# Optimization experiments

Measured on AMD Instinct MI355X. Metric: run time of the kernel, lower is better.

## Reference

```python
import jax, jax.numpy as jnp
import numpy as np

N, E, H = 50000, 800000, 128
NUM_NC = 40
NUM_LAYERS = 3


def setup_inputs() -> dict:
    key = jax.random.key(0)
    ks = jax.random.split(key, 16)
    s = 1.0 / np.sqrt(H)
    inp = {
        "x": jax.random.normal(ks[0], (N, H), jnp.float32),
        "edge_index": jax.random.randint(ks[1], (2, E), 0, N, jnp.int64),
        "na_alphas": 0.001 * jax.random.normal(ks[2], (3, 4), jnp.float32),
        "sc_alphas": 0.001 * jax.random.normal(ks[3], (2, 2), jnp.float32),
        "la_alphas": 0.001 * jax.random.normal(ks[4], (1, 3), jnp.float32),
        "lin1_W": s * jax.random.normal(ks[5], (H, H), jnp.float32),
        "lin1_b": jnp.zeros((H,), jnp.float32),
        "gcn_W": s * jax.random.normal(ks[6], (3, H, H), jnp.float32),
        "gcn_b": jnp.zeros((3, H), jnp.float32),
        "sage_Ws": s * jax.random.normal(ks[7], (3, H, H), jnp.float32),
        "sage_Wn": s * jax.random.normal(ks[8], (3, H, H), jnp.float32),
        "gin_W": s * jax.random.normal(ks[9], (3, H, H), jnp.float32),
        "gin_b": jnp.zeros((3, H), jnp.float32),
        "gin_eps": jnp.zeros((3,), jnp.float32),
        "gat_W": s * jax.random.normal(ks[10], (3, H, H), jnp.float32),
        "gat_as": s * jax.random.normal(ks[11], (3, H), jnp.float32),
        "gat_ad": s * jax.random.normal(ks[12], (3, H), jnp.float32),
        "nc_W": s * jax.random.normal(ks[13], (NUM_NC, H), jnp.float32),
        "nc_b": jnp.zeros((NUM_NC,), jnp.float32),
    }
    return inp


def _gcn(x, src, dst, deg_inv_sqrt, W, b):
    h = x @ W.T + b                           # [N, H]
    norm = deg_inv_sqrt[src] * deg_inv_sqrt[dst]
    msg = h[src] * norm[:, None]              # [E, H] gather
    return jax.ops.segment_sum(msg, dst, num_segments=N)


def _sage(x, src, dst, deg, Ws, Wn):
    agg = jax.ops.segment_sum(x[src], dst, num_segments=N) / jnp.maximum(deg, 1.0)[:, None]
    return x @ Ws.T + agg @ Wn.T


def _gin(x, src, dst, W, b, eps):
    agg = jax.ops.segment_sum(x[src], dst, num_segments=N)
    return ((1.0 + eps) * x + agg) @ W.T + b


def _gat(x, src, dst, W, a_s, a_d):
    h = x @ W.T                               # [N, H]
    logits = jax.nn.leaky_relu((h @ a_s)[src] + (h @ a_d)[dst], 0.2)  # [E]
    m = jax.ops.segment_max(logits, dst, num_segments=N)
    e = jnp.exp(logits - m[dst])
    z = jax.ops.segment_sum(e, dst, num_segments=N)
    alpha = e / (z[dst] + 1e-16)
    return jax.ops.segment_sum(alpha[:, None] * h[src], dst, num_segments=N)


def _na_mixed(x, w, src, dst, deg, dis, l, gcn_W, gcn_b, sage_Ws, sage_Wn,
              gin_W, gin_b, gin_eps, gat_W, gat_as, gat_ad):
    # sum_i w_i * elu(op_i(x, edge_index))
    o0 = _gcn(x, src, dst, dis, gcn_W[l], gcn_b[l])
    o1 = _sage(x, src, dst, deg, sage_Ws[l], sage_Wn[l])
    o2 = _gin(x, src, dst, gin_W[l], gin_b[l], gin_eps[l])
    o3 = _gat(x, src, dst, gat_W[l], gat_as[l], gat_ad[l])
    return (w[0] * jax.nn.elu(o0) + w[1] * jax.nn.elu(o1)
            + w[2] * jax.nn.elu(o2) + w[3] * jax.nn.elu(o3))


def reference(x, edge_index, na_alphas, sc_alphas, la_alphas, lin1_W, lin1_b,
              gcn_W, gcn_b, sage_Ws, sage_Wn, gin_W, gin_b, gin_eps,
              gat_W, gat_as, gat_ad, nc_W, nc_b):
    src, dst = edge_index[0], edge_index[1]
    deg = jax.ops.segment_sum(jnp.ones((E,), x.dtype), dst, num_segments=N)
    dis = jnp.where(deg > 0, 1.0 / jnp.sqrt(jnp.maximum(deg, 1.0)), 0.0)

    na_w = jax.nn.softmax(na_alphas, axis=-1)   # [3, 4]
    sc_w = jax.nn.softmax(sc_alphas, axis=-1)   # [2, 2] (none, skip)
    la_w = jax.nn.softmax(la_alphas, axis=-1)   # [1, 3]

    h = x @ lin1_W.T + lin1_b                   # dropout: eval mode -> identity
    xs = []
    cur = h
    for l in range(NUM_LAYERS):
        cur = _na_mixed(cur, na_w[l], src, dst, deg, dis, l, gcn_W, gcn_b,
                        sage_Ws, sage_Wn, gin_W, gin_b, gin_eps,
                        gat_W, gat_as, gat_ad)
        xs.append(cur)
    x1, x2, x3 = xs

    # fix_last=True: x4 = (x3, sc0(x1), sc1(x2)); SC ops = {none->0, skip->id}
    t = jnp.stack([x3, sc_w[0, 1] * x1, sc_w[1, 1] * x2], axis=0)  # [3, N, H]

    # layer aggregator: sum_i w_i * relu(op_i(tuple)); ops = {max, mean, sum}
    x5 = (la_w[0, 0] * jax.nn.relu(jnp.max(t, axis=0))
          + la_w[0, 1] * jax.nn.relu(jnp.mean(t, axis=0))
          + la_w[0, 2] * jax.nn.relu(jnp.sum(t, axis=0)))

    return x5 @ nc_W.T + nc_b                   # [N, NUM_NC]
```

## Files before the change

kernel.cpp:

```cpp
#include <hip/hip_runtime.h>
#include <hip/hip_bf16.h>

typedef unsigned short u16;
typedef unsigned int u32;
typedef __attribute__((ext_vector_type(8))) short short8;
typedef __attribute__((ext_vector_type(4))) float f32x4;
typedef __attribute__((ext_vector_type(2))) float f32x2;

#define HD 128
#define ETILE 8192

__device__ inline float b2f(u16 u){ u32 v = ((u32)u) << 16; return __uint_as_float(v); }
__device__ inline u16 f2b(float f){
  u32 u = __float_as_uint(f);
  u32 r = (u + 0x7fffu + ((u >> 16) & 1u)) >> 16;
  return (u16)r;
}
__device__ inline u32 pack2(float a, float b){
  __hip_bfloat162 h = __float22bfloat162_rn(make_float2(a, b));
  union { __hip_bfloat162 h; u32 u; } c; c.h = h; return c.u;
}
__device__ inline float lo2f(u32 w){ return b2f((u16)(w & 0xffff)); }
__device__ inline float hi2f(u32 w){ return b2f((u16)(w >> 16)); }
__device__ inline float eluf(float x){ return x > 0.f ? x : __expf(x) - 1.f; }
__device__ inline float reluf(float x){ return x > 0.f ? x : 0.f; }
__device__ inline float sane(float x){
  if (!(x == x)) return 0.f;
  return fminf(fmaxf(x, -1e30f), 1e30f);
}
__device__ inline u32 fenc(float f){ u32 u = __float_as_uint(f); return (u & 0x80000000u) ? ~u : (u | 0x80000000u); }
__device__ inline float fdec(u32 u){ return __uint_as_float((u & 0x80000000u) ? (u & 0x7fffffffu) : ~u); }
__device__ __forceinline__ void async16(const u16* g, u16* l){
  __builtin_amdgcn_global_load_lds((const __attribute__((address_space(1))) void*)g,
                                   (__attribute__((address_space(3))) void*)l, 16, 0, 0);
}

__global__ void k_small(const float* __restrict__ na_a, const float* __restrict__ sc_a,
                        const float* __restrict__ la_a, const float* __restrict__ gatW,
                        const float* __restrict__ gat_as, const float* __restrict__ gat_ad,
                        const float* __restrict__ gin_eps, float* __restrict__ sm,
                        u32* __restrict__ maxs)
{
  int t = threadIdx.x;
  if (t < 3) maxs[t] = 0u;
  if (t == 0){
    for (int l = 0; l < 3; l++){
      float a[4]; float mx = -1e30f;
      for (int i = 0; i < 4; i++){ a[i] = na_a[l*4+i]; mx = fmaxf(mx, a[i]); }
      float ssum = 0.f;
      for (int i = 0; i < 4; i++){ a[i] = __expf(a[i]-mx); ssum += a[i]; }
      for (int i = 0; i < 4; i++) sm[l*4+i] = a[i]/ssum;
    }
    for (int r = 0; r < 2; r++){
      float a0 = sc_a[r*2], a1 = sc_a[r*2+1];
      float mx = fmaxf(a0,a1);
      float e0 = __expf(a0-mx), e1 = __expf(a1-mx);
      sm[12+r] = e1/(e0+e1);
    }
    {
      float a0=la_a[0], a1=la_a[1], a2=la_a[2];
      float mx = fmaxf(fmaxf(a0,a1),a2);
      float e0=__expf(a0-mx), e1=__expf(a1-mx), e2=__expf(a2-mx);
      float ssum = e0+e1+e2;
      sm[14]=e0/ssum; sm[15]=e1/ssum; sm[16]=e2/ssum;
    }
    for (int l=0;l<3;l++) sm[17+l] = 1.f + gin_eps[l];
  }
  if (t < 128){
    for (int l=0;l<3;l++){
      float a1=0.f, a2=0.f;
      for (int k=0;k<128;k++){
        float wv = gatW[l*16384 + k*128 + t];
        a1 = fmaf(wv, gat_as[l*128+k], a1);
        a2 = fmaf(wv, gat_ad[l*128+k], a2);
      }
      sm[32  + l*128 + t] = a1;
      sm[416 + l*128 + t] = a2;
    }
  }
}

__device__ __forceinline__ uint4 cvt8(const float* __restrict__ p){
  float4 v0 = *(const float4*)p;
  float4 v1 = *(const float4*)(p + 4);
  uint4 o;
  o.x = pack2(v0.x, v0.y);
  o.y = pack2(v0.z, v0.w);
  o.z = pack2(v1.x, v1.y);
  o.w = pack2(v1.z, v1.w);
  return o;
}
__global__ void k_wcvt(const float* __restrict__ lin1W, const float* __restrict__ gcnW,
                       const float* __restrict__ Ws, const float* __restrict__ Wn,
                       const float* __restrict__ ginW, const float* __restrict__ gatW,
                       u16* __restrict__ wsb)
{
  int i = blockIdx.x*256 + threadIdx.x;
  if (i >= 32768) return;
  int m = i >> 11;
  int j = i & 2047;
  int r = j >> 4, c = j & 15;
  const float* src;
  if (m == 0)       src = lin1W;
  else if (m < 4)   src = gcnW + (m-1)*16384;
  else if (m < 7)   src = Ws   + (m-4)*16384;
  else if (m < 10)  src = Wn   + (m-7)*16384;
  else if (m < 13)  src = ginW + (m-10)*16384;
  else              src = gatW + (m-13)*16384;
  int dj = r*16 + (c ^ (r & 15));
  *(uint4*)(wsb + ((size_t)m*2048 + dj)*8) = cvt8(src + r*HD + c*8);
}


__global__ void k_ehist(const int* __restrict__ ei, int E, int* __restrict__ eh){
  __shared__ int h[256];
  int t = threadIdx.x, b = blockIdx.x;
  h[t] = 0; __syncthreads();
  int base = b*ETILE;
  #pragma unroll
  for (int r = 0; r < ETILE/256; r++){
    int e = base + r*256 + t;
    if (e < E) atomicAdd(&h[ei[E + e] >> 8], 1);
  }
  __syncthreads();
  eh[b*256 + t] = h[t];
}
__global__ void k_escan(int* __restrict__ eh, int nblk, int* __restrict__ btot){
  __shared__ int s[256];
  int b = blockIdx.x, t = threadIdx.x;
  int carry = 0;
  int rounds = (nblk + 255)/256;
  for (int r = 0; r < rounds; r++){
    int i = r*256 + t;
    int v = (i < nblk) ? eh[i*256 + b] : 0;
    s[t] = v; __syncthreads();
    for (int off = 1; off < 256; off <<= 1){
      int a = (t >= off) ? s[t - off] : 0;
      __syncthreads();
      s[t] += a;
      __syncthreads();
    }
    if (i < nblk) eh[i*256 + b] = s[t] - v + carry;
    carry += s[255];
    __syncthreads();
  }
  if (t == 0) btot[b] = carry;
}
__global__ void k_bscan(const int* __restrict__ btot, int B, int E, int* __restrict__ bbase){
  __shared__ int s[256];
  int t = threadIdx.x;
  int v = (t < B) ? btot[t] : 0;
  s[t] = v; __syncthreads();
  for (int off = 1; off < 256; off <<= 1){
    int a = (t >= off) ? s[t - off] : 0;
    __syncthreads();
    s[t] += a;
    __syncthreads();
  }
  if (t < B) bbase[t] = s[t] - v;
  if (t == 0) bbase[B] = E;
}
__global__ void k_escat(const int* __restrict__ ei, int E, int B,
                        const int* __restrict__ eh, const int* __restrict__ bbase,
                        int2* __restrict__ ebuf){
  __shared__ int cur[256];
  int t = threadIdx.x, b = blockIdx.x;
  cur[t] = (t < B) ? bbase[t] + eh[b*256 + t] : 0;
  __syncthreads();
  int base = b*ETILE;
  #pragma unroll
  for (int r = 0; r < ETILE/256; r++){
    int e = base + r*256 + t;
    if (e < E){
      int sv = ei[e], dv = ei[E + e];
      int p = atomicAdd(&cur[dv >> 8], 1);
      ebuf[p] = make_int2(sv, dv);
    }
  }
}
__global__ void k_bcount(const int2* __restrict__ ebuf, const int* __restrict__ bbase,
                         int Nn, int* __restrict__ cnt){
  __shared__ int c[256];
  int t = threadIdx.x, b = blockIdx.x;
  c[t] = 0; __syncthreads();
  int beg = bbase[b], end2 = bbase[b+1];
  for (int i = beg + t; i < end2; i += 256)
    atomicAdd(&c[ebuf[i].y & 255], 1);
  __syncthreads();
  int node = b*256 + t;
  if (node < Nn) cnt[node] = c[t];
}
__global__ void k_bfill(const int2* __restrict__ ebuf, const int* __restrict__ bbase,
                        const int* __restrict__ rowptr, int Nn, int* __restrict__ csr){
  __shared__ int cu[256];
  int t = threadIdx.x, b = blockIdx.x;
  int node = b*256 + t;
  cu[t] = (node < Nn) ? rowptr[node] : 0;
  __syncthreads();
  int beg = bbase[b], end2 = bbase[b+1];
  for (int i = beg + t; i < end2; i += 256){
    int2 ed = ebuf[i];
    int p = atomicAdd(&cu[ed.y & 255], 1);
    csr[p] = ed.x;
  }
}

__global__ void k_scan1(const int* __restrict__ cnt, int Nn, int* __restrict__ bsum){
  __shared__ int red[256];
  int b = blockIdx.x, t = threadIdx.x;
  int base = b*1024 + t*4;
  int s = 0;
  #pragma unroll
  for (int k = 0; k < 4; k++){ int i = base + k; if (i < Nn) s += cnt[i]; }
  red[t] = s; __syncthreads();
  for (int off = 128; off; off >>= 1){
    if (t < off) red[t] += red[t + off];
    __syncthreads();
  }
  if (t == 0) bsum[b] = red[0];
}

__global__ void k_scan2(const int* __restrict__ bsum, int nb,
                        int* __restrict__ boffs, int* __restrict__ rowptr, int Nn){
  __shared__ int sc[1024];
  int t = threadIdx.x;
  int own = (t < nb) ? bsum[t] : 0;
  sc[t] = own;
  __syncthreads();
  for (int off = 1; off < 1024; off <<= 1){
    int add = (t >= off) ? sc[t - off] : 0;
    __syncthreads();
    sc[t] += add;
    __syncthreads();
  }
  if (t < nb) boffs[t] = sc[t] - own;
  if (t == 1023) rowptr[Nn] = sc[1023];
}

__global__ void k_scan3(const int* __restrict__ cnt, const int* __restrict__ boffs, int Nn,
                        int* __restrict__ rowptr, float4* __restrict__ nd){
  __shared__ int red[256];
  int b = blockIdx.x, t = threadIdx.x;
  int base = b*1024 + t*4;
  int c[4]; int s = 0;
  #pragma unroll
  for (int k = 0; k < 4; k++){ int i = base + k; c[k] = (i < Nn) ? cnt[i] : 0; s += c[k]; }
  red[t] = s; __syncthreads();
  for (int off = 1; off < 256; off <<= 1){
    int add = (t >= off) ? red[t - off] : 0;
    __syncthreads();
    red[t] += add;
    __syncthreads();
  }
  int run = red[t] - s + boffs[b];
  #pragma unroll
  for (int k = 0; k < 4; k++){
    int i = base + k;
    if (i < Nn){
      rowptr[i] = run;
      float f = (float)c[k];
      nd[i].z = c[k] > 0 ? 1.f/sqrtf(f) : 0.f;
      nd[i].w = 1.f/fmaxf(f, 1.f);
      run += c[k];
    }
  }
}

__global__ void k_histblk(const int* __restrict__ cnt, int Nn, int* __restrict__ bh){
  __shared__ int h[256];
  int t = threadIdx.x, b = blockIdx.x;
  h[t] = 0; __syncthreads();
  int base = b*1024;
  #pragma unroll
  for (int k = 0; k < 4; k++){
    int i = base + t + k*256;
    if (i < Nn){ int d = cnt[i]; if (d > 255) d = 255; atomicAdd(&h[d], 1); }
  }
  __syncthreads();
  bh[b*256 + t] = h[t];
}
__global__ void k_hsscan(int* __restrict__ bh, int nb){
  __shared__ int tot[256];
  __shared__ int sc[256];
  int t = threadIdx.x;
  int s = 0;
  for (int b = 0; b < nb; b++){
    int v = bh[b*256 + t];
    bh[b*256 + t] = s;
    s += v;
  }
  tot[t] = s;
  int rt = 255 - t;
  __syncthreads();
  sc[rt] = tot[t];
  __syncthreads();
  for (int off = 1; off < 256; off <<= 1){
    int a = (rt >= off) ? sc[rt - off] : 0;
    __syncthreads();
    sc[rt] += a;
    __syncthreads();
  }
  int binbase = sc[rt] - tot[t];
  for (int b = 0; b < nb; b++) bh[b*256 + t] += binbase;
}
__global__ void k_permscat(const int* __restrict__ cnt, int Nn,
                           const int* __restrict__ bh, int* __restrict__ perm){
  __shared__ int cur[256];
  int t = threadIdx.x, b = blockIdx.x;
  cur[t] = bh[b*256 + t];
  __syncthreads();
  int base = b*1024;
  #pragma unroll
  for (int k = 0; k < 4; k++){
    int i = base + t + k*256;
    if (i < Nn){
      int d = cnt[i]; if (d > 255) d = 255;
      int p = atomicAdd(&cur[d], 1);
      perm[p] = i;
    }
  }
}

__global__ __launch_bounds__(256)
void k_agg(const u16* __restrict__ X, const int* __restrict__ rowptr, const int* __restrict__ csr,
           const int* __restrict__ perm,
           const float4* __restrict__ nd, const float* __restrict__ sm,
           const u32* __restrict__ maxs, int layer, int Nn,
           u16* __restrict__ Qb, u16* __restrict__ Pm, u16* __restrict__ Gb, u16* __restrict__ Rb,
           float* __restrict__ b0)
{
  int tid = threadIdx.x;
  int lane = tid & 63;
  int g = lane >> 4, t = lane & 15;
  int idx = blockIdx.x*16 + (tid >> 6)*4 + g;
  if (idx >= Nn) return;
  int wv = perm[idx];
  int beg = rowptr[wv], end = rowptr[wv+1];
  float4 ndw = nd[wv];
  float dval = ndw.y;
  float bnd = fdec(maxs[layer]) + dval;
  float mloc = fmaxf(bnd, 0.2f*bnd);
  f32x2 p2[4], q2[4], r2[4];
  #pragma unroll
  for (int k = 0; k < 4; k++){ p2[k] = (f32x2){0.f,0.f}; q2[k] = (f32x2){0.f,0.f}; r2[k] = (f32x2){0.f,0.f}; }
  float z = 0.f, qd = 0.f;
  int e = beg;
  int nsv0=0, nsv1=0, nsv2=0, nsv3=0;
  if (e + 3 < end){ nsv0 = csr[e]; nsv1 = csr[e+1]; nsv2 = csr[e+2]; nsv3 = csr[e+3]; }
  while (e + 3 < end){
    int sv0 = nsv0, sv1 = nsv1, sv2 = nsv2, sv3 = nsv3;
    int en = e + 4;
    if (en + 3 < end){ nsv0 = csr[en]; nsv1 = csr[en+1]; nsv2 = csr[en+2]; nsv3 = csr[en+3]; }
    float4 n0 = nd[sv0], n1 = nd[sv1], n2 = nd[sv2], n3 = nd[sv3];
    uint4 xv0 = *(const uint4*)(X + (size_t)sv0*HD + (t ^ (sv0 & 15))*8);
    uint4 xv1 = *(const uint4*)(X + (size_t)sv1*HD + (t ^ (sv1 & 15))*8);
    uint4 xv2 = *(const uint4*)(X + (size_t)sv2*HD + (t ^ (sv2 & 15))*8);
    uint4 xv3 = *(const uint4*)(X + (size_t)sv3*HD + (t ^ (sv3 & 15))*8);
    float s0 = n0.x + dval, s1 = n1.x + dval, s2 = n2.x + dval, s3 = n3.x + dval;
    float lg0 = fmaxf(s0, 0.2f*s0), lg1 = fmaxf(s1, 0.2f*s1);
    float lg2 = fmaxf(s2, 0.2f*s2), lg3 = fmaxf(s3, 0.2f*s3);
    float ew0 = __expf(lg0 - mloc), ew1 = __expf(lg1 - mloc);
    float ew2 = __expf(lg2 - mloc), ew3 = __expf(lg3 - mloc);
    u32 a0[4] = {xv0.x, xv0.y, xv0.z, xv0.w};
    u32 a1[4] = {xv1.x, xv1.y, xv1.z, xv1.w};
    u32 a2[4] = {xv2.x, xv2.y, xv2.z, xv2.w};
    u32 a3[4] = {xv3.x, xv3.y, xv3.z, xv3.w};
    f32x2 d0 = {n0.z, n0.z}, d1 = {n1.z, n1.z}, d2 = {n2.z, n2.z}, d3 = {n3.z, n3.z};
    f32x2 e0 = {ew0, ew0}, e1v = {ew1, ew1}, e2v = {ew2, ew2}, e3v = {ew3, ew3};
    #pragma unroll
    for (int k = 0; k < 4; k++){
      f32x2 xf0 = {lo2f(a0[k]), hi2f(a0[k])};
      f32x2 xf1 = {lo2f(a1[k]), hi2f(a1[k])};
      f32x2 xf2 = {lo2f(a2[k]), hi2f(a2[k])};
      f32x2 xf3 = {lo2f(a3[k]), hi2f(a3[k])};
      p2[k] += (xf0 + xf1) + (xf2 + xf3);
      q2[k] = __builtin_elementwise_fma(xf0, d0, q2[k]);
      q2[k] = __builtin_elementwise_fma(xf1, d1, q2[k]);
      q2[k] = __builtin_elementwise_fma(xf2, d2, q2[k]);
      q2[k] = __builtin_elementwise_fma(xf3, d3, q2[k]);
      r2[k] = __builtin_elementwise_fma(xf0, e0, r2[k]);
      r2[k] = __builtin_elementwise_fma(xf1, e1v, r2[k]);
      r2[k] = __builtin_elementwise_fma(xf2, e2v, r2[k]);
      r2[k] = __builtin_elementwise_fma(xf3, e3v, r2[k]);
    }
    z += (ew0 + ew1) + (ew2 + ew3);
    qd += (n0.z + n1.z) + (n2.z + n3.z);
    e = en;
  }
  if (e + 1 < end){
    int sv0 = csr[e], sv1 = csr[e+1];
    float4 n0 = nd[sv0], n1 = nd[sv1];
    uint4 xv0 = *(const uint4*)(X + (size_t)sv0*HD + (t ^ (sv0 & 15))*8);
    uint4 xv1 = *(const uint4*)(X + (size_t)sv1*HD + (t ^ (sv1 & 15))*8);
    float s0 = n0.x + dval, s1 = n1.x + dval;
    float lg0 = fmaxf(s0, 0.2f*s0);
    float lg1 = fmaxf(s1, 0.2f*s1);
    float ew0 = __expf(lg0 - mloc), ew1 = __expf(lg1 - mloc);
    u32 a0[4] = {xv0.x, xv0.y, xv0.z, xv0.w};
    u32 a1[4] = {xv1.x, xv1.y, xv1.z, xv1.w};
    f32x2 d0 = {n0.z, n0.z}, d1 = {n1.z, n1.z};
    f32x2 e0 = {ew0, ew0},   e1v = {ew1, ew1};
    #pragma unroll
    for (int k = 0; k < 4; k++){
      f32x2 xf0 = {lo2f(a0[k]), hi2f(a0[k])};
      f32x2 xf1 = {lo2f(a1[k]), hi2f(a1[k])};
      p2[k] += xf0 + xf1;
      q2[k] = __builtin_elementwise_fma(xf0, d0, q2[k]);
      q2[k] = __builtin_elementwise_fma(xf1, d1, q2[k]);
      r2[k] = __builtin_elementwise_fma(xf0, e0, r2[k]);
      r2[k] = __builtin_elementwise_fma(xf1, e1v, r2[k]);
    }
    z += ew0 + ew1; qd += n0.z + n1.z;
    e += 2;
  }
  if (e < end){
    int sv = csr[e];
    float4 n0 = nd[sv];
    uint4 xv = *(const uint4*)(X + (size_t)sv*HD + (t ^ (sv & 15))*8);
    float s = n0.x + dval;
    float lg = fmaxf(s, 0.2f*s);
    float ew = __expf(lg - mloc);
    u32 a0[4] = {xv.x, xv.y, xv.z, xv.w};
    f32x2 d0 = {n0.z, n0.z}, e0 = {ew, ew};
    #pragma unroll
    for (int k = 0; k < 4; k++){
      f32x2 xf = {lo2f(a0[k]), hi2f(a0[k])};
      p2[k] += xf;
      q2[k] = __builtin_elementwise_fma(xf, d0, q2[k]);
      r2[k] = __builtin_elementwise_fma(xf, e0, r2[k]);
    }
    z += ew; qd += n0.z;
  }
  {
    float disv = ndw.z, dinvv = ndw.w;
    float zinv = 1.f/(z + 1e-16f);
    float e1 = sm[17 + layer];
    int tch = t ^ (wv & 15);
    size_t o = (size_t)wv*HD + tch*8;
    uint4 xo = *(const uint4*)(X + o);
    u32 ax[4] = {xo.x, xo.y, xo.z, xo.w};
    uint4 qo, po, go, ro;
    u32* qp = (u32*)&qo; u32* pp = (u32*)&po; u32* gp = (u32*)&go; u32* rp = (u32*)&ro;
    #pragma unroll
    for (int k = 0; k < 4; k++){
      float x0 = lo2f(ax[k]), x1 = hi2f(ax[k]);
      qp[k] = pack2(disv*q2[k].x, disv*q2[k].y);
      pp[k] = pack2(dinvv*p2[k].x, dinvv*p2[k].y);
      gp[k] = pack2(fmaf(e1, x0, p2[k].x), fmaf(e1, x1, p2[k].y));
      rp[k] = pack2(zinv*r2[k].x, zinv*r2[k].y);
    }
    *(uint4*)(Qb + o) = qo;
    *(uint4*)(Pm + o) = po;
    *(uint4*)(Gb + o) = go;
    *(uint4*)(Rb + o) = ro;
    if (t == 0) b0[wv] = disv*qd;
  }
}

__device__ __forceinline__ void stageB_async(u16* lds, const u16* __restrict__ w, int tid){
  int lane = tid & 63, wave = tid >> 6;
  #pragma unroll
  for (int i = 0; i < 8; i++){
    int cb = wave*64 + 256*i;
    async16(w + (size_t)(cb + lane)*8, lds + (size_t)cb*8);
  }
}
__device__ __forceinline__ void stageA64_async(u16* lds, const u16* __restrict__ src,
                                               int mbase, int Nn, int tid){
  int lane = tid & 63, wave = tid >> 6;
  #pragma unroll
  for (int i = 0; i < 4; i++){
    int cb = wave*64 + 256*i;
    int gr = mbase + ((cb + lane) >> 4);
    if (gr < Nn)
      async16(src + ((size_t)mbase*16 + cb + lane)*8, lds + (size_t)cb*8);
  }
}
__device__ __forceinline__ void stageA64_f32(u16* lds, const float* __restrict__ src,
                                             int mbase, int Nn, int tid){
  #pragma unroll
  for (int i = 0; i < 4; i++){
    int chunk = tid + 256*i;
    int r = chunk >> 4;
    int c = chunk & 15;
    uint4 v = {0u,0u,0u,0u};
    int gr = mbase + r;
    if (gr < Nn) v = cvt8(src + (size_t)gr*HD + c*8);
    *(uint4*)(lds + (r*16 + (c ^ (r & 15)))*8) = v;
  }
}
__device__ __forceinline__ void mfma_tile64(const u16* Als, const u16* Bls,
                                            int m0, int lane, f32x4 acc[8]){
  int quad = lane >> 4, lr = lane & 15;
  #pragma unroll
  for (int ks = 0; ks < 4; ks++){
    int q = ks*4 + quad;
    short8 a, b[8];
    int row = m0 + lr;
    a = *(const short8*)(Als + (row*16 + (q ^ lr))*8);
    #pragma unroll
    for (int ct = 0; ct < 8; ct++){
      int brow = ct*16 + lr;
      b[ct] = *(const short8*)(Bls + (brow*16 + (q ^ lr))*8);
    }
    #pragma unroll
    for (int ct = 0; ct < 8; ct++)
      acc[ct] = __builtin_amdgcn_mfma_f32_16x16x32_bf16(a, b[ct], acc[ct], 0, 0, 0);
  }
}

__global__ __launch_bounds__(256,3)
void k_gemm1(const float* __restrict__ A, const u16* __restrict__ Wb, const float* __restrict__ bias,
             const float* __restrict__ sm, float4* __restrict__ nd, u32* __restrict__ maxs,
             int Nn, u16* __restrict__ out)
{
  __shared__ __align__(16) u16 Als[64*128];
  __shared__ __align__(16) u16 Bls[128*128];
  __shared__ float mred[4];
  int tid = threadIdx.x;
  int lane = tid & 63, wave = tid >> 6;
  int m0 = wave*16, mbase = blockIdx.x*64;
  int quad = lane >> 4, lr = lane & 15;
  f32x4 acc[8];
  #pragma unroll
  for (int ct=0;ct<8;ct++) acc[ct] = (f32x4){0.f,0.f,0.f,0.f};
  stageB_async(Bls, Wb, tid);
  stageA64_f32(Als, A, mbase, Nn, tid);
  __syncthreads();
  mfma_tile64(Als, Bls, m0, lane, acc);
  #pragma unroll
  for (int ct=0;ct<8;ct++){
    float bc = bias[ct*16+lr];
    #pragma unroll
    for (int r=0;r<4;r++) acc[ct][r] = sane(acc[ct][r] + bc);
  }
  #pragma unroll
  for (int ct=0;ct<8;ct++){
    int c2 = ct*2 + (lr >> 3);
    #pragma unroll
    for (int r=0;r<4;r++){
      int grow = mbase + m0 + quad*4 + r;
      if (grow < Nn) out[(size_t)grow*HD + (c2 ^ (grow & 15))*8 + (lr & 7)] = f2b(acc[ct][r]);
    }
  }
  {
    const float* wsv = sm + 32;
    const float* wdv = sm + 416;
    float sp[4] = {0.f,0.f,0.f,0.f}, dp[4] = {0.f,0.f,0.f,0.f};
    #pragma unroll
    for (int ct=0;ct<8;ct++){
      float wsc = wsv[ct*16+lr], wdc = wdv[ct*16+lr];
      #pragma unroll
      for (int r=0;r<4;r++){
        sp[r] = fmaf(acc[ct][r], wsc, sp[r]);
        dp[r] = fmaf(acc[ct][r], wdc, dp[r]);
      }
    }
    #pragma unroll
    for (int off=1; off<16; off<<=1)
      #pragma unroll
      for (int r=0;r<4;r++){ sp[r] += __shfl_xor(sp[r], off); dp[r] += __shfl_xor(dp[r], off); }
    float ms = -3.4e38f;
    #pragma unroll
    for (int r=0;r<4;r++){
      int grow = mbase + m0 + quad*4 + r;
      if (grow < Nn){
        ms = fmaxf(ms, sp[r]);
        if (lr == 0) *(float2*)&nd[grow] = make_float2(sp[r], dp[r]);
      }
    }
    ms = fmaxf(ms, __shfl_xor(ms, 16));
    ms = fmaxf(ms, __shfl_xor(ms, 32));
    if (lane == 0) mred[wave] = ms;
    __syncthreads();
    if (tid == 0){
      float m = fmaxf(fmaxf(mred[0],mred[1]), fmaxf(mred[2],mred[3]));
      atomicMax(maxs + 0, fenc(m));
    }
  }
}

__global__ __launch_bounds__(256,3)
void k_layer3(const u16* __restrict__ X, const u16* __restrict__ Qb,
              const u16* __restrict__ Pm, const u16* __restrict__ Gb, const u16* __restrict__ Rb,
              float4* __restrict__ nd, const float* __restrict__ b0,
              const u16* __restrict__ wsb,
              const float* __restrict__ gcnB, const float* __restrict__ ginB,
              const float* __restrict__ sm, u32* __restrict__ maxs,
              int layer, int Nn, u16* __restrict__ out)
{
  __shared__ __align__(16) u16 At[64*128];
  __shared__ __align__(16) u16 Bt[128*128];
  __shared__ float mred[4];
  int tid = threadIdx.x;
  int lane = tid & 63, wave = tid >> 6;
  int m0 = wave*16, mbase = blockIdx.x*64;
  int quad = lane >> 4, lr = lane & 15;
  float w0 = sm[layer*4+0], w1 = sm[layer*4+1], w2 = sm[layer*4+2], w3 = sm[layer*4+3];
  const u16* gcnWb = wsb + (size_t)(1  + layer)*16384;
  const u16* WsWb  = wsb + (size_t)(4  + layer)*16384;
  const u16* WnWb  = wsb + (size_t)(7  + layer)*16384;
  const u16* ginWb = wsb + (size_t)(10 + layer)*16384;
  const u16* gatWb = wsb + (size_t)(13 + layer)*16384;

  f32x4 mix[8];
  f32x4 acc[8];
  float b0r[4];
  #pragma unroll
  for (int r=0;r<4;r++){
    int grow = mbase + m0 + quad*4 + r;
    b0r[r] = (grow < Nn) ? b0[grow] : 0.f;
  }

  stageB_async(Bt, gcnWb, tid);
  stageA64_async(At, Qb, mbase, Nn, tid);
  __syncthreads();
  #pragma unroll
  for (int ct=0;ct<8;ct++) acc[ct] = (f32x4){0.f,0.f,0.f,0.f};
  mfma_tile64(At, Bt, m0, lane, acc);
  {
    float gb[8];
    #pragma unroll
    for (int ct=0;ct<8;ct++) gb[ct] = gcnB[layer*HD + ct*16+lr];
    #pragma unroll
    for (int ct=0;ct<8;ct++)
      #pragma unroll
      for (int r=0;r<4;r++)
        mix[ct][r] = w0 * eluf(acc[ct][r] + b0r[r]*gb[ct]);
  }
  __syncthreads();

  stageB_async(Bt, WsWb, tid);
  stageA64_async(At, X, mbase, Nn, tid);
  __syncthreads();
  #pragma unroll
  for (int ct=0;ct<8;ct++) acc[ct] = (f32x4){0.f,0.f,0.f,0.f};
  mfma_tile64(At, Bt, m0, lane, acc);
  __syncthreads();
  stageB_async(Bt, WnWb, tid);
  stageA64_async(At, Pm, mbase, Nn, tid);
  __syncthreads();
  mfma_tile64(At, Bt, m0, lane, acc);
  #pragma unroll
  for (int ct=0;ct<8;ct++)
    #pragma unroll
    for (int r=0;r<4;r++)
      mix[ct][r] += w1 * eluf(acc[ct][r]);
  __syncthreads();

  stageB_async(Bt, ginWb, tid);
  stageA64_async(At, Gb, mbase, Nn, tid);
  __syncthreads();
  #pragma unroll
  for (int ct=0;ct<8;ct++) acc[ct] = (f32x4){0.f,0.f,0.f,0.f};
  mfma_tile64(At, Bt, m0, lane, acc);
  {
    float gib[8];
    #pragma unroll
    for (int ct=0;ct<8;ct++) gib[ct] = ginB[layer*HD + ct*16+lr];
    #pragma unroll
    for (int ct=0;ct<8;ct++)
      #pragma unroll
      for (int r=0;r<4;r++)
        mix[ct][r] += w2 * eluf(acc[ct][r] + gib[ct]);
  }
  __syncthreads();

  stageB_async(Bt, gatWb, tid);
  stageA64_async(At, Rb, mbase, Nn, tid);
  __syncthreads();
  #pragma unroll
  for (int ct=0;ct<8;ct++) acc[ct] = (f32x4){0.f,0.f,0.f,0.f};
  mfma_tile64(At, Bt, m0, lane, acc);
  #pragma unroll
  for (int ct=0;ct<8;ct++)
    #pragma unroll
    for (int r=0;r<4;r++)
      mix[ct][r] = sane(mix[ct][r] + w3 * eluf(acc[ct][r]));

  #pragma unroll
  for (int ct=0;ct<8;ct++){
    int c2 = ct*2 + (lr >> 3);
    #pragma unroll
    for (int r=0;r<4;r++){
      int grow = mbase + m0 + quad*4 + r;
      if (grow < Nn) out[(size_t)grow*HD + (c2 ^ (grow & 15))*8 + (lr & 7)] = f2b(mix[ct][r]);
    }
  }
  if (layer < 2){
    const float* wsv = sm + 32  + (layer+1)*128;
    const float* wdv = sm + 416 + (layer+1)*128;
    float sp[4] = {0.f,0.f,0.f,0.f}, dp[4] = {0.f,0.f,0.f,0.f};
    #pragma unroll
    for (int ct=0;ct<8;ct++){
      float wsc = wsv[ct*16+lr], wdc = wdv[ct*16+lr];
      #pragma unroll
      for (int r=0;r<4;r++){
        sp[r] = fmaf(mix[ct][r], wsc, sp[r]);
        dp[r] = fmaf(mix[ct][r], wdc, dp[r]);
      }
    }
    #pragma unroll
    for (int off=1; off<16; off<<=1)
      #pragma unroll
      for (int r=0;r<4;r++){ sp[r] += __shfl_xor(sp[r], off); dp[r] += __shfl_xor(dp[r], off); }
    float ms = -3.4e38f;
    #pragma unroll
    for (int r=0;r<4;r++){
      int grow = mbase + m0 + quad*4 + r;
      if (grow < Nn){
        ms = fmaxf(ms, sp[r]);
        if (lr == 0) *(float2*)&nd[grow] = make_float2(sp[r], dp[r]);
      }
    }
    ms = fmaxf(ms, __shfl_xor(ms, 16));
    ms = fmaxf(ms, __shfl_xor(ms, 32));
    if (lane == 0) mred[wave] = ms;
    __syncthreads();
    if (tid == 0){
      float m = fmaxf(fmaxf(mred[0],mred[1]), fmaxf(mred[2],mred[3]));
      atomicMax(maxs + layer + 1, fenc(m));
    }
  }
}

__global__ __launch_bounds__(256)
void k_nc(const u16* __restrict__ X1, const u16* __restrict__ X2, const u16* __restrict__ X3,
          const float* __restrict__ W, const float* __restrict__ bias,
          const float* __restrict__ sm, int Nn, float* __restrict__ out)
{
  __shared__ __align__(16) u16 xs[32*136];
  __shared__ __align__(16) float wn[40*132];
  __shared__ float bs[40];
  int t = threadIdx.x;
  int nb = blockIdx.x*32;
  float c1 = sm[12], c2 = sm[13], la0 = sm[14], la1 = sm[15], la2 = sm[16];
  #pragma unroll
  for (int i = 0; i < 2; i++){
    int chunk = t + 256*i;
    int r = chunk >> 4, c = chunk & 15;
    uint4 v = {0u,0u,0u,0u};
    int gr = nb + r;
    if (gr < Nn){
      size_t o = (size_t)gr*HD + ((c ^ (gr & 15))*8);
      uint4 u1 = *(const uint4*)(X1 + o);
      uint4 u2 = *(const uint4*)(X2 + o);
      uint4 u3 = *(const uint4*)(X3 + o);
      u32* u1p = (u32*)&u1; u32* u2p = (u32*)&u2; u32* u3p = (u32*)&u3; u32* vp = (u32*)&v;
      #pragma unroll
      for (int k = 0; k < 4; k++){
        float o0, o1;
        {
          float a1 = lo2f(u1p[k]), a2 = lo2f(u2p[k]), a3 = lo2f(u3p[k]);
          float t0 = a3, t1 = c1*a1, t2 = c2*a2;
          float smm = t0 + t1 + t2;
          float mx = fmaxf(fmaxf(t0,t1),t2);
          o0 = la0*reluf(mx) + la1*reluf(smm*(1.f/3.f)) + la2*reluf(smm);
        }
        {
          float a1 = hi2f(u1p[k]), a2 = hi2f(u2p[k]), a3 = hi2f(u3p[k]);
          float t0 = a3, t1 = c1*a1, t2 = c2*a2;
          float smm = t0 + t1 + t2;
          float mx = fmaxf(fmaxf(t0,t1),t2);
          o1 = la0*reluf(mx) + la1*reluf(smm*(1.f/3.f)) + la2*reluf(smm);
        }
        vp[k] = pack2(sane(o0), sane(o1));
      }
    }
    *(uint4*)(xs + r*136 + c*8) = v;
  }
  #pragma unroll
  for (int i = 0; i < 5; i++){
    int chunk = t + 256*i;
    int r = chunk >> 5, c = chunk & 31;
    *(float4*)(wn + r*132 + c*4) = *(const float4*)(W + r*HD + c*4);
  }
  if (t < 40) bs[t] = bias[t];
  __syncthreads();
  int nl = t >> 3, cg = t & 7;
  float acc[5];
  #pragma unroll
  for (int j = 0; j < 5; j++) acc[j] = bs[cg + 8*j];
  for (int k = 0; k < 128; k++){
    float xv = b2f(xs[nl*136 + k]);
    #pragma unroll
    for (int j = 0; j < 5; j++)
      acc[j] = fmaf(xv, wn[(cg + 8*j)*132 + k], acc[j]);
  }
  int gr = nb + nl;
  if (gr < Nn){
    #pragma unroll
    for (int j = 0; j < 5; j++)
      out[(size_t)gr*40 + cg + 8*j] = sane(acc[j]);
  }
}

extern "C" void kernel_launch(void* const* d_in, const int* in_sizes, int n_in,
                              void* d_out, int out_size, void* d_ws, size_t ws_size,
                              hipStream_t stream)
{
  (void)n_in; (void)out_size; (void)ws_size;
  const int N = in_sizes[0] / HD;
  const int E = in_sizes[1] / 2;
  const float* x      = (const float*)d_in[0];
  const int*   ei     = (const int*)d_in[1];
  const float* na_a   = (const float*)d_in[2];
  const float* sc_a   = (const float*)d_in[3];
  const float* la_a   = (const float*)d_in[4];
  const float* lin1W  = (const float*)d_in[5];
  const float* lin1b  = (const float*)d_in[6];
  const float* gcnW   = (const float*)d_in[7];
  const float* gcnB   = (const float*)d_in[8];
  const float* sageWs = (const float*)d_in[9];
  const float* sageWn = (const float*)d_in[10];
  const float* ginW   = (const float*)d_in[11];
  const float* ginB   = (const float*)d_in[12];
  const float* ginE   = (const float*)d_in[13];
  const float* gatW   = (const float*)d_in[14];
  const float* gatAs  = (const float*)d_in[15];
  const float* gatAd  = (const float*)d_in[16];
  const float* ncW    = (const float*)d_in[17];
  const float* ncB    = (const float*)d_in[18];

  char* base = (char*)d_ws;
  size_t off = 0;
  auto alloc = [&](size_t b) -> void* {
    void* p = base + off;
    off += (b + 255) & ~(size_t)255;
    return p;
  };
  const int NB  = (N + 1023) / 1024;
  const int B   = (N + 255) >> 8;
  const int nbe = (E + ETILE - 1) / ETILE;
  float*  smalls = (float*)alloc(4096);
  u32*    maxs   = (u32*)alloc(256);
  int*    cnt    = (int*)alloc((size_t)N*4);
  int*    rowptr = (int*)alloc(((size_t)N+1)*4);
  int*    bsum   = (int*)alloc(4096);
  int*    boffs  = (int*)alloc(4096);
  int*    bh     = (int*)alloc((size_t)NB*256*4);
  int*    perm   = (int*)alloc((size_t)N*4);
  int*    eh     = (int*)alloc((size_t)nbe*256*4);
  int*    btot   = (int*)alloc(1024);
  int*    bbase  = (int*)alloc(1040);
  float4* nd     = (float4*)alloc((size_t)N*16);
  float*  b0     = (float*)alloc((size_t)N*4);
  int*    csr    = (int*)alloc((size_t)E*4);
  u16*    wsb    = (u16*)alloc((size_t)16*16384*2);
  u16*    xh     = (u16*)alloc((size_t)N*HD*2);
  u16*    x1     = (u16*)alloc((size_t)N*HD*2);
  u16*    x2     = (u16*)alloc((size_t)N*HD*2);
  u16*    Qb     = (u16*)alloc((size_t)N*HD*2);
  u16*    Pm     = (u16*)alloc((size_t)N*HD*2);
  u16*    Gb     = (u16*)alloc((size_t)N*HD*2);
  u16*    Rb     = (u16*)alloc((size_t)N*HD*2);
  int2*   ebuf   = (int2*)Qb;

  k_small<<<1,128,0,stream>>>(na_a, sc_a, la_a, gatW, gatAs, gatAd, ginE, smalls, maxs);
  k_wcvt<<<128,256,0,stream>>>(lin1W, gcnW, sageWs, sageWn, ginW, gatW, wsb);
  k_ehist<<<nbe,256,0,stream>>>(ei, E, eh);
  k_escan<<<B,256,0,stream>>>(eh, nbe, btot);
  k_bscan<<<1,256,0,stream>>>(btot, B, E, bbase);
  k_escat<<<nbe,256,0,stream>>>(ei, E, B, eh, bbase, ebuf);
  k_bcount<<<B,256,0,stream>>>(ebuf, bbase, N, cnt);
  k_histblk<<<NB,256,0,stream>>>(cnt, N, bh);
  k_hsscan<<<1,256,0,stream>>>(bh, NB);
  k_permscat<<<NB,256,0,stream>>>(cnt, N, bh, perm);
  k_scan1<<<NB,256,0,stream>>>(cnt, N, bsum);
  k_scan2<<<1,1024,0,stream>>>(bsum, NB, boffs, rowptr, N);
  k_scan3<<<NB,256,0,stream>>>(cnt, boffs, N, rowptr, nd);
  k_bfill<<<B,256,0,stream>>>(ebuf, bbase, rowptr, N, csr);
  int gbl64 = (N + 63)/64;
  k_gemm1<<<gbl64,256,0,stream>>>(x, wsb, lin1b, smalls, nd, maxs, N, xh);
  const u16* xc = xh;
  u16* outs[3] = {x1, x2, xh};
  int abl = (N + 15)/16;
  for (int l = 0; l < 3; l++){
    k_agg<<<abl,256,0,stream>>>(xc, rowptr, csr, perm, nd, smalls, maxs, l, N, Qb, Pm, Gb, Rb, b0);
    k_layer3<<<gbl64,256,0,stream>>>(xc, Qb, Pm, Gb, Rb, nd, b0, wsb,
                                     gcnB, ginB, smalls, maxs, l, N, outs[l]);
    xc = outs[l];
  }
  int ncbl = (N + 31)/32;
  k_nc<<<ncbl,256,0,stream>>>(x1, x2, xh, ncW, ncB, smalls, N, (float*)d_out);
}
```

Baseline: 467.2 us.

## Load GEMM operands directly from global memory into registers in layer kernel

The per-layer mixed-op kernel no longer stages A tiles and weight matrices through LDS with barriers. Each wave now loads its A rows and the B fragments straight from global memory (weights served by L1/L2) and prefetches the next operand's A fragment into registers while the current MFMA chain runs. This removes shared-memory traffic and the many __syncthreads calls, and frees LDS for higher occupancy. In exchange every wave re-reads the full weight matrices from cache and uses more registers.

```diff
diff --git a/kernel.cpp b/kernel.cpp
--- a/kernel.cpp
+++ b/kernel.cpp
@@ -465,17 +465,6 @@
     async16(w + (size_t)(cb + lane)*8, lds + (size_t)cb*8);
   }
 }
-__device__ __forceinline__ void stageA64_async(u16* lds, const u16* __restrict__ src,
-                                               int mbase, int Nn, int tid){
-  int lane = tid & 63, wave = tid >> 6;
-  #pragma unroll
-  for (int i = 0; i < 4; i++){
-    int cb = wave*64 + 256*i;
-    int gr = mbase + ((cb + lane) >> 4);
-    if (gr < Nn)
-      async16(src + ((size_t)mbase*16 + cb + lane)*8, lds + (size_t)cb*8);
-  }
-}
 __device__ __forceinline__ void stageA64_f32(u16* lds, const float* __restrict__ src,
                                              int mbase, int Nn, int tid){
   #pragma unroll
@@ -589,8 +578,6 @@
               const float* __restrict__ sm, u32* __restrict__ maxs,
               int layer, int Nn, u16* __restrict__ out)
 {
-  __shared__ __align__(16) u16 At[64*128];
-  __shared__ __align__(16) u16 Bt[128*128];
   __shared__ float mred[4];
   int tid = threadIdx.x;
   int lane = tid & 63, wave = tid >> 6;
@@ -603,6 +590,13 @@
   const u16* ginWb = wsb + (size_t)(10 + layer)*16384;
   const u16* gatWb = wsb + (size_t)(13 + layer)*16384;
 
+  int arow = mbase + m0 + lr; if (arow >= Nn) arow = Nn - 1;
+  size_t abase = (size_t)arow * HD;
+  int co[4];
+  #pragma unroll
+  for (int ks = 0; ks < 4; ks++) co[ks] = ((ks*4 + quad) ^ lr) * 8;
+  int bro = lr * 128;
+
   f32x4 mix[8];
   f32x4 acc[8];
   float b0r[4];
@@ -612,12 +606,24 @@
     b0r[r] = (grow < Nn) ? b0[grow] : 0.f;
   }
 
-  stageB_async(Bt, gcnWb, tid);
-  stageA64_async(At, Qb, mbase, Nn, tid);
-  __syncthreads();
+  short8 a0[4], a1[4];
+  #pragma unroll
+  for (int ks=0;ks<4;ks++) a0[ks] = *(const short8*)(Qb + abase + co[ks]);
+  #pragma unroll
+  for (int ks=0;ks<4;ks++) a1[ks] = *(const short8*)(X + abase + co[ks]);
+
   #pragma unroll
   for (int ct=0;ct<8;ct++) acc[ct] = (f32x4){0.f,0.f,0.f,0.f};
-  mfma_tile64(At, Bt, m0, lane, acc);
+  #pragma unroll
+  for (int ks=0;ks<4;ks++){
+    #pragma unroll
+    for (int ct=0;ct<8;ct++){
+      short8 b = *(const short8*)(gcnWb + ct*2048 + bro + co[ks]);
+      acc[ct] = __builtin_amdgcn_mfma_f32_16x16x32_bf16(a0[ks], b, acc[ct], 0, 0, 0);
+    }
+  }
+  #pragma unroll
+  for (int ks=0;ks<4;ks++) a0[ks] = *(const short8*)(Pm + abase + co[ks]);
   {
     float gb[8];
     #pragma unroll
@@ -628,32 +634,45 @@
       for (int r=0;r<4;r++)
         mix[ct][r] = w0 * eluf(acc[ct][r] + b0r[r]*gb[ct]);
   }
-  __syncthreads();
-
-  stageB_async(Bt, WsWb, tid);
-  stageA64_async(At, X, mbase, Nn, tid);
-  __syncthreads();
+
   #pragma unroll
   for (int ct=0;ct<8;ct++) acc[ct] = (f32x4){0.f,0.f,0.f,0.f};
-  mfma_tile64(At, Bt, m0, lane, acc);
-  __syncthreads();
-  stageB_async(Bt, WnWb, tid);
-  stageA64_async(At, Pm, mbase, Nn, tid);
-  __syncthreads();
-  mfma_tile64(At, Bt, m0, lane, acc);
+  #pragma unroll
+  for (int ks=0;ks<4;ks++){
+    #pragma unroll
+    for (int ct=0;ct<8;ct++){
+      short8 b = *(const short8*)(WsWb + ct*2048 + bro + co[ks]);
+      acc[ct] = __builtin_amdgcn_mfma_f32_16x16x32_bf16(a1[ks], b, acc[ct], 0, 0, 0);
+    }
+  }
+  #pragma unroll
+  for (int ks=0;ks<4;ks++) a1[ks] = *(const short8*)(Gb + abase + co[ks]);
+  #pragma unroll
+  for (int ks=0;ks<4;ks++){
+    #pragma unroll
+    for (int ct=0;ct<8;ct++){
+      short8 b = *(const short8*)(WnWb + ct*2048 + bro + co[ks]);
+      acc[ct] = __builtin_amdgcn_mfma_f32_16x16x32_bf16(a0[ks], b, acc[ct], 0, 0, 0);
+    }
+  }
+  #pragma unroll
+  for (int ks=0;ks<4;ks++) a0[ks] = *(const short8*)(Rb + abase + co[ks]);
   #pragma unroll
   for (int ct=0;ct<8;ct++)
     #pragma unroll
     for (int r=0;r<4;r++)
       mix[ct][r] += w1 * eluf(acc[ct][r]);
-  __syncthreads();
-
-  stageB_async(Bt, ginWb, tid);
-  stageA64_async(At, Gb, mbase, Nn, tid);
-  __syncthreads();
+
   #pragma unroll
   for (int ct=0;ct<8;ct++) acc[ct] = (f32x4){0.f,0.f,0.f,0.f};
-  mfma_tile64(At, Bt, m0, lane, acc);
+  #pragma unroll
+  for (int ks=0;ks<4;ks++){
+    #pragma unroll
+    for (int ct=0;ct<8;ct++){
+      short8 b = *(const short8*)(ginWb + ct*2048 + bro + co[ks]);
+      acc[ct] = __builtin_amdgcn_mfma_f32_16x16x32_bf16(a1[ks], b, acc[ct], 0, 0, 0);
+    }
+  }
   {
     float gib[8];
     #pragma unroll
@@ -664,14 +683,17 @@
       for (int r=0;r<4;r++)
         mix[ct][r] += w2 * eluf(acc[ct][r] + gib[ct]);
   }
-  __syncthreads();
-
-  stageB_async(Bt, gatWb, tid);
-  stageA64_async(At, Rb, mbase, Nn, tid);
-  __syncthreads();
+
   #pragma unroll
   for (int ct=0;ct<8;ct++) acc[ct] = (f32x4){0.f,0.f,0.f,0.f};
-  mfma_tile64(At, Bt, m0, lane, acc);
+  #pragma unroll
+  for (int ks=0;ks<4;ks++){
+    #pragma unroll
+    for (int ct=0;ct<8;ct++){
+      short8 b = *(const short8*)(gatWb + ct*2048 + bro + co[ks]);
+      acc[ct] = __builtin_amdgcn_mfma_f32_16x16x32_bf16(a0[ks], b, acc[ct], 0, 0, 0);
+    }
+  }
   #pragma unroll
   for (int ct=0;ct<8;ct++)
     #pragma unroll
```

Measured after the change: 512.1 us. +9.6%, slower.
